# Performance work log

Measured on AMD Instinct MI355X. Metric: run time of the kernel, lower is better.

Reference implementation:

```python
import jax, jax.numpy as jnp
import numpy as np

B, S, H, NH = 2, 2048, 1024, 16
DH = H // NH
FF = 4 * H
EPS = 1e-5


def setup_inputs() -> dict:
    key = jax.random.key(0)
    ks = jax.random.split(key, 16)
    sd = 0.02
    inp = {
        "x": jax.random.normal(ks[0], (B, S, H), dtype=jnp.float32),
        "Wq": jax.random.normal(ks[1], (H, H), dtype=jnp.float32) * sd,
        "bq": jnp.zeros((H,), jnp.float32),
        "Wk": jax.random.normal(ks[2], (H, H), dtype=jnp.float32) * sd,
        "bk": jnp.zeros((H,), jnp.float32),
        "Wv": jax.random.normal(ks[3], (H, H), dtype=jnp.float32) * sd,
        "bv": jnp.zeros((H,), jnp.float32),
        "Wo": jax.random.normal(ks[4], (H, H), dtype=jnp.float32) * sd,
        "bo": jnp.zeros((H,), jnp.float32),
        "W1": jax.random.normal(ks[5], (H, FF), dtype=jnp.float32) * sd,
        "b1": jnp.zeros((FF,), jnp.float32),
        "W2": jax.random.normal(ks[6], (FF, H), dtype=jnp.float32) * sd,
        "b2": jnp.zeros((H,), jnp.float32),
        "g1": jnp.ones((H,), jnp.float32),
        "be1": jnp.zeros((H,), jnp.float32),
        "g2": jnp.ones((H,), jnp.float32),
        "be2": jnp.zeros((H,), jnp.float32),
    }
    return inp


def _layernorm(x, g, b):
    mu = jnp.mean(x, axis=-1, keepdims=True)
    var = jnp.mean(jnp.square(x - mu), axis=-1, keepdims=True)
    return (x - mu) * jax.lax.rsqrt(var + EPS) * g + b


def _block(x, Wq, bq, Wk, bk, Wv, bv, Wo, bo, W1, b1, W2, b2, g1, be1, g2, be2):
    # pre-LN attention
    h = _layernorm(x, g1, be1)
    q = (h @ Wq + bq).reshape(B, S, NH, DH)
    k = (h @ Wk + bk).reshape(B, S, NH, DH)
    v = (h @ Wv + bv).reshape(B, S, NH, DH)
    scale = DH ** -0.5
    scores = jnp.einsum("bqhd,bkhd->bhqk", q, k) * scale  # [B,NH,S,S]
    causal = jnp.tril(jnp.ones((S, S), dtype=bool))
    scores = jnp.where(causal, scores, -jnp.inf)
    attn = jax.nn.softmax(scores, axis=-1)
    out = jnp.einsum("bhqk,bkhd->bqhd", attn, v).reshape(B, S, H)
    x = x + (out @ Wo + bo)
    # pre-LN FFN with exact GELU (torch nn.GELU default)
    h = _layernorm(x, g2, be2)
    h = jax.nn.gelu(h @ W1 + b1, approximate=False)
    return x + (h @ W2 + b2)


def reference(x, Wq, bq, Wk, bk, Wv, bv, Wo, bo, W1, b1, W2, b2, g1, be1, g2, be2):
    return _block(x, Wq, bq, Wk, bk, Wv, bv, Wo, bo, W1, b1, W2, b2, g1, be1, g2, be2)
```

## Files before the change

### kernel.cpp

```cpp
#include <hip/hip_runtime.h>
#include <cstdint>
#include <cstddef>

typedef unsigned short u16;
typedef __attribute__((ext_vector_type(8))) __bf16 bf16v8;
typedef __attribute__((ext_vector_type(8))) unsigned short u16x8;
typedef __attribute__((ext_vector_type(4))) float f32x4;

constexpr int Bc = 2, Sc = 2048, Hc = 1024, NHc = 16, DHc = 64, FFc = 4096;
constexpr int Mc = Bc * Sc;

__device__ __forceinline__ u16 f2bf(float f) {
  unsigned u = __builtin_bit_cast(unsigned, f);
  return (u16)((u + 0x7FFFu + ((u >> 16) & 1u)) >> 16);
}

__device__ __forceinline__ int xcd_swz(int bid, int n) {
  const int q = n >> 3;
  return (bid & 7) * q + (bid >> 3);
}

__device__ __forceinline__ void gload_lds16(const void* g, void* l) {
  __builtin_amdgcn_global_load_lds(
      (const __attribute__((address_space(1))) unsigned*)(uintptr_t)g,
      (__attribute__((address_space(3))) unsigned*)(unsigned)(uintptr_t)l,
      16, 0, 0);
}

struct WP4 { const float* w0; const float* w1; const float* w2; const float* w3; };
__global__ __launch_bounds__(256) void wconv4_kernel(WP4 p, u16* __restrict__ Wt) {
  __shared__ float tile[64][65];
  const float* W = (blockIdx.z == 0) ? p.w0 : (blockIdx.z == 1) ? p.w1
                  : (blockIdx.z == 2) ? p.w2 : p.w3;
  u16* dst = Wt + (size_t)blockIdx.z * 1024 * 1024;
  const int n0 = blockIdx.x << 6, k0 = blockIdx.y << 6;
  const int t = threadIdx.x;
  const int col = t & 63, r0 = t >> 6;
#pragma unroll
  for (int i = 0; i < 16; ++i) {
    int r = (i << 2) + r0;
    tile[r][col] = W[(size_t)(k0 + r) * 1024 + n0 + col];
  }
  __syncthreads();
#pragma unroll
  for (int i = 0; i < 16; ++i) {
    int n = (i << 2) + r0;
    dst[(size_t)(n0 + n) * 1024 + k0 + col] = f2bf(tile[col][n]);
  }
}

struct WP2 { const float* w1; const float* w2; };
__global__ __launch_bounds__(256) void wconv12_kernel(WP2 p, u16* __restrict__ d1,
                                                      u16* __restrict__ d2) {
  __shared__ float tile[64][65];
  const int z = blockIdx.z;
  const float* W = z ? p.w2 : p.w1;
  u16* dst = z ? d2 : d1;
  const int K = z ? 4096 : 1024, N = z ? 1024 : 4096;
  const int nb = N >> 6;
  const int n0 = (blockIdx.x % nb) << 6, k0 = (blockIdx.x / nb) << 6;
  const int t = threadIdx.x;
  const int col = t & 63, r0 = t >> 6;
#pragma unroll
  for (int i = 0; i < 16; ++i) {
    int r = (i << 2) + r0;
    tile[r][col] = W[(size_t)(k0 + r) * N + n0 + col];
  }
  __syncthreads();
#pragma unroll
  for (int i = 0; i < 16; ++i) {
    int n = (i << 2) + r0;
    dst[(size_t)(n0 + n) * K + k0 + col] = f2bf(tile[col][n]);
  }
}

__global__ __launch_bounds__(256) void ln_kernel(const float* __restrict__ x,
                                                 const float* __restrict__ g,
                                                 const float* __restrict__ be,
                                                 u16* __restrict__ y) {
  const int row = blockIdx.x;
  const int t = threadIdx.x;
  const float4 v = ((const float4*)(x + (size_t)row * Hc))[t];
  float s1 = v.x + v.y + v.z + v.w;
  float s2 = v.x * v.x + v.y * v.y + v.z * v.z + v.w * v.w;
#pragma unroll
  for (int o = 32; o > 0; o >>= 1) {
    s1 += __shfl_xor(s1, o);
    s2 += __shfl_xor(s2, o);
  }
  __shared__ float r1[4], r2[4];
  const int wave = t >> 6, lane = t & 63;
  if (lane == 0) { r1[wave] = s1; r2[wave] = s2; }
  __syncthreads();
  s1 = r1[0] + r1[1] + r1[2] + r1[3];
  s2 = r2[0] + r2[1] + r2[2] + r2[3];
  const float mu = s1 * (1.f / Hc);
  const float var = s2 * (1.f / Hc) - mu * mu;
  const float rs = rsqrtf(var + 1e-5f);
  const float4 gv = ((const float4*)g)[t];
  const float4 bv = ((const float4*)be)[t];
  ushort4 ov;
  ov.x = f2bf((v.x - mu) * rs * gv.x + bv.x);
  ov.y = f2bf((v.y - mu) * rs * gv.y + bv.y);
  ov.z = f2bf((v.z - mu) * rs * gv.z + bv.z);
  ov.w = f2bf((v.w - mu) * rs * gv.w + bv.w);
  ((ushort4*)(y + (size_t)row * Hc))[t] = ov;
}

template <int EPI>
__global__ __launch_bounds__(256, 2) void gemm_kernel(
    const u16* __restrict__ A, const u16* __restrict__ Bt,
    const float* __restrict__ bias, const float* __restrict__ res,
    u16* __restrict__ outb, float* __restrict__ outf,
    int N, int Kext, int lda, int ldb, int nx) {
  __shared__ __align__(16) char smraw[32768];
  u16 (*As)[128][32] = (u16(*)[128][32])smraw;
  u16 (*Bs)[128][32] = (u16(*)[128][32])(smraw + 16384);
  float (*Cs)[16][132] = (float(*)[16][132])smraw;

  const int t = threadIdx.x;
  const int wave = t >> 6, lane = t & 63;
  const int pid = xcd_swz(blockIdx.x, gridDim.x);
  const int bn = pid % nx, bm = pid / nx;
  const int wm = wave >> 1, wn = wave & 1;
  const int fr = lane & 15, fk = (lane >> 4) << 3;

  f32x4 acc[4][4] = {};

  const int srow = (wave << 4) + (lane >> 2);
  const int scol = (lane & 3) << 3;
  const u16* Ag0 = A + (size_t)(bm * 128 + srow) * lda + scol;
  const u16* Ag1 = Ag0 + (size_t)64 * lda;
  const u16* Bg0 = Bt + (size_t)(bn * 128 + srow) * ldb + scol;
  const u16* Bg1 = Bg0 + (size_t)64 * ldb;

  const int nk = Kext >> 5;
  auto STAGE = [&](int buf, int k0) {
    gload_lds16(Ag0 + k0, &As[buf][wave << 4][0]);
    gload_lds16(Ag1 + k0, &As[buf][64 + (wave << 4)][0]);
    gload_lds16(Bg0 + k0, &Bs[buf][wave << 4][0]);
    gload_lds16(Bg1 + k0, &Bs[buf][64 + (wave << 4)][0]);
  };

  STAGE(0, 0);
  int cur = 0;
  for (int kt = 0; kt < nk; ++kt) {
    if (kt + 1 < nk) {
      STAGE(cur ^ 1, (kt + 1) << 5);
      asm volatile("s_waitcnt vmcnt(4)" ::: "memory");
    } else {
      asm volatile("s_waitcnt vmcnt(0)" ::: "memory");
    }
    __builtin_amdgcn_s_barrier();
    bf16v8 af[4], bfr[4];
#pragma unroll
    for (int i = 0; i < 4; ++i) af[i] = *(const bf16v8*)&As[cur][(wm << 6) + (i << 4) + fr][fk];
#pragma unroll
    for (int j = 0; j < 4; ++j) bfr[j] = *(const bf16v8*)&Bs[cur][(wn << 6) + (j << 4) + fr][fk];
    asm volatile("s_waitcnt lgkmcnt(0)" ::: "memory");
    __builtin_amdgcn_s_barrier();
    __builtin_amdgcn_s_setprio(1);
#pragma unroll
    for (int i = 0; i < 4; ++i)
#pragma unroll
      for (int j = 0; j < 4; ++j)
        acc[i][j] = __builtin_amdgcn_mfma_f32_16x16x32_bf16(af[i], bfr[j], acc[i][j], 0, 0, 0);
    __builtin_amdgcn_s_setprio(0);
    cur ^= 1;
  }
  __syncthreads();

  const int cr = (lane >> 4) << 2, cc = lane & 15;
  const int b2 = t >> 7, u = t & 127, lr = u >> 3, c0 = (u & 7) << 4;

  for (int i = 0; i < 4; ++i) {
#pragma unroll
    for (int j = 0; j < 4; ++j) {
      int col = (wn << 6) + (j << 4) + cc;
      float bz = bias[(bn << 7) + col];
#pragma unroll
      for (int r = 0; r < 4; ++r) Cs[wm][cr + r][col] = acc[i][j][r] + bz;
    }
    __syncthreads();
    {
      const float* crow = &Cs[b2][lr][c0];
      f32x4 v0 = *(const f32x4*)(crow);
      f32x4 v1 = *(const f32x4*)(crow + 4);
      f32x4 v2 = *(const f32x4*)(crow + 8);
      f32x4 v3 = *(const f32x4*)(crow + 12);
      const int grow = (bm << 7) + (b2 << 6) + (i << 4) + lr;
      const int gc = (bn << 7) + c0;
      const size_t base = (size_t)grow * N + gc;
      if constexpr (EPI == 0 || EPI == 1) {
        float vv[16];
#pragma unroll
        for (int k = 0; k < 4; ++k) { vv[k] = v0[k]; vv[4 + k] = v1[k]; vv[8 + k] = v2[k]; vv[12 + k] = v3[k]; }
        if constexpr (EPI == 1) {
#pragma unroll
          for (int k = 0; k < 16; ++k)
            vv[k] = 0.5f * vv[k] * (1.0f + erff(vv[k] * 0.70710678118654752f));
        }
        u16x8 o0, o1;
#pragma unroll
        for (int k = 0; k < 8; ++k) { o0[k] = f2bf(vv[k]); o1[k] = f2bf(vv[8 + k]); }
        *(u16x8*)&outb[base] = o0;
        *(u16x8*)&outb[base + 8] = o1;
      } else {
        const f32x4* rp = (const f32x4*)&res[base];
        v0 += rp[0]; v1 += rp[1]; v2 += rp[2]; v3 += rp[3];
        f32x4* op = (f32x4*)&outf[base];
        op[0] = v0; op[1] = v1; op[2] = v2; op[3] = v3;
      }
    }
    __syncthreads();
  }
}

template <int EPI>
__global__ __launch_bounds__(256, 2) void gemm_p_kernel(
    const u16* __restrict__ A, const u16* __restrict__ Bt,
    const float* __restrict__ bias, const float* __restrict__ res,
    u16* __restrict__ outb, float* __restrict__ outf,
    int N, int Kext, int lda, int ldb, int nx) {
  __shared__ __align__(16) char smraw[49152];
  u16 (*As)[128][32] = (u16(*)[128][32])smraw;
  u16 (*Bs)[128][32] = (u16(*)[128][32])(smraw + 24576);
  float (*Cs)[16][132] = (float(*)[16][132])smraw;

  const int t = threadIdx.x;
  const int wave = t >> 6, lane = t & 63;
  const int pid = xcd_swz(blockIdx.x, gridDim.x);
  const int bn = pid % nx, bm = pid / nx;
  const int wm = wave >> 1, wn = wave & 1;
  const int fr = lane & 15, fk = (lane >> 4) << 3;

  f32x4 acc[4][4] = {};

  const int srow = (wave << 4) + (lane >> 2);
  const int scol = (lane & 3) << 3;
  const u16* Ag0 = A + (size_t)(bm * 128 + srow) * lda + scol;
  const u16* Ag1 = Ag0 + (size_t)64 * lda;
  const u16* Bg0 = Bt + (size_t)(bn * 128 + srow) * ldb + scol;
  const u16* Bg1 = Bg0 + (size_t)64 * ldb;

  const int nk = Kext >> 5;
  auto STAGE = [&](int buf, int k0) {
    gload_lds16(Ag0 + k0, &As[buf][wave << 4][0]);
    gload_lds16(Ag1 + k0, &As[buf][64 + (wave << 4)][0]);
    gload_lds16(Bg0 + k0, &Bs[buf][wave << 4][0]);
    gload_lds16(Bg1 + k0, &Bs[buf][64 + (wave << 4)][0]);
  };

  STAGE(0, 0);
  STAGE(1, 32);
  int cur = 0;
  for (int kt = 0; kt < nk; ++kt) {
    if (kt + 2 < nk) {
      int sb = cur + 2; if (sb >= 3) sb -= 3;
      STAGE(sb, (kt + 2) << 5);
      asm volatile("s_waitcnt vmcnt(8)" ::: "memory");
    } else if (kt + 1 < nk) {
      asm volatile("s_waitcnt vmcnt(4)" ::: "memory");
    } else {
      asm volatile("s_waitcnt vmcnt(0)" ::: "memory");
    }
    __builtin_amdgcn_s_barrier();
    bf16v8 af[4], bfr[4];
#pragma unroll
    for (int i = 0; i < 4; ++i) af[i] = *(const bf16v8*)&As[cur][(wm << 6) + (i << 4) + fr][fk];
#pragma unroll
    for (int j = 0; j < 4; ++j) bfr[j] = *(const bf16v8*)&Bs[cur][(wn << 6) + (j << 4) + fr][fk];
    asm volatile("s_waitcnt lgkmcnt(0)" ::: "memory");
    __builtin_amdgcn_s_barrier();
    __builtin_amdgcn_s_setprio(1);
#pragma unroll
    for (int i = 0; i < 4; ++i)
#pragma unroll
      for (int j = 0; j < 4; ++j)
        acc[i][j] = __builtin_amdgcn_mfma_f32_16x16x32_bf16(af[i], bfr[j], acc[i][j], 0, 0, 0);
    __builtin_amdgcn_s_setprio(0);
    cur = (cur + 1 == 3) ? 0 : cur + 1;
  }
  __syncthreads();

  const int cr = (lane >> 4) << 2, cc = lane & 15;
  const int b2 = t >> 7, u = t & 127, lr = u >> 3, c0 = (u & 7) << 4;

  for (int i = 0; i < 4; ++i) {
#pragma unroll
    for (int j = 0; j < 4; ++j) {
      int col = (wn << 6) + (j << 4) + cc;
      float bz = bias[(bn << 7) + col];
#pragma unroll
      for (int r = 0; r < 4; ++r) Cs[wm][cr + r][col] = acc[i][j][r] + bz;
    }
    __syncthreads();
    {
      const float* crow = &Cs[b2][lr][c0];
      f32x4 v0 = *(const f32x4*)(crow);
      f32x4 v1 = *(const f32x4*)(crow + 4);
      f32x4 v2 = *(const f32x4*)(crow + 8);
      f32x4 v3 = *(const f32x4*)(crow + 12);
      const int grow = (bm << 7) + (b2 << 6) + (i << 4) + lr;
      const int gc = (bn << 7) + c0;
      const size_t base = (size_t)grow * N + gc;
      if constexpr (EPI == 0 || EPI == 1) {
        float vv[16];
#pragma unroll
        for (int k = 0; k < 4; ++k) { vv[k] = v0[k]; vv[4 + k] = v1[k]; vv[8 + k] = v2[k]; vv[12 + k] = v3[k]; }
        if constexpr (EPI == 1) {
#pragma unroll
          for (int k = 0; k < 16; ++k)
            vv[k] = 0.5f * vv[k] * (1.0f + erff(vv[k] * 0.70710678118654752f));
        }
        u16x8 o0, o1;
#pragma unroll
        for (int k = 0; k < 8; ++k) { o0[k] = f2bf(vv[k]); o1[k] = f2bf(vv[8 + k]); }
        *(u16x8*)&outb[base] = o0;
        *(u16x8*)&outb[base + 8] = o1;
      } else {
        const f32x4* rp = (const f32x4*)&res[base];
        v0 += rp[0]; v1 += rp[1]; v2 += rp[2]; v3 += rp[3];
        f32x4* op = (f32x4*)&outf[base];
        op[0] = v0; op[1] = v1; op[2] = v2; op[3] = v3;
      }
    }
    __syncthreads();
  }
}

__global__ __launch_bounds__(256, 2) void qkv_gemm_kernel(
    const u16* __restrict__ A, const u16* __restrict__ Bt,
    const float* __restrict__ bq, const float* __restrict__ bk,
    const float* __restrict__ bv,
    u16* __restrict__ Qb, u16* __restrict__ Kb, u16* __restrict__ Vtg) {
  constexpr int K = 1024;
  __shared__ __align__(16) char smraw[49152];
  u16 (*As)[128][32] = (u16(*)[128][32])smraw;
  u16 (*Bs)[128][32] = (u16(*)[128][32])(smraw + 24576);
  float (*Cs)[16][132] = (float(*)[16][132])smraw;

  const int t = threadIdx.x;
  const int wave = t >> 6, lane = t & 63;
  const int pid = xcd_swz(blockIdx.x, 768);
  const int bn = pid % 24, bm = pid / 24;
  const int wm = wave >> 1, wn = wave & 1;
  const int fr = lane & 15, fk = (lane >> 4) << 3;
  const int seg = bn >> 3;

  f32x4 acc[4][4] = {};

  const int srow = (wave << 4) + (lane >> 2);
  const int scol = (lane & 3) << 3;
  const u16* Ag0 = A + (size_t)(bm * 128 + srow) * K + scol;
  const u16* Ag1 = Ag0 + (size_t)64 * K;
  const u16* Bg0 = Bt + (size_t)(bn * 128 + srow) * K + scol;
  const u16* Bg1 = Bg0 + (size_t)64 * K;

  const int nk = K >> 5;
  auto STAGE = [&](int buf, int k0) {
    gload_lds16(Ag0 + k0, &As[buf][wave << 4][0]);
    gload_lds16(Ag1 + k0, &As[buf][64 + (wave << 4)][0]);
    gload_lds16(Bg0 + k0, &Bs[buf][wave << 4][0]);
    gload_lds16(Bg1 + k0, &Bs[buf][64 + (wave << 4)][0]);
  };

  STAGE(0, 0);
  STAGE(1, 32);
  int cur = 0;
  for (int kt = 0; kt < nk; ++kt) {
    if (kt + 2 < nk) {
      int sb = cur + 2; if (sb >= 3) sb -= 3;
      STAGE(sb, (kt + 2) << 5);
      asm volatile("s_waitcnt vmcnt(8)" ::: "memory");
    } else if (kt + 1 < nk) {
      asm volatile("s_waitcnt vmcnt(4)" ::: "memory");
    } else {
      asm volatile("s_waitcnt vmcnt(0)" ::: "memory");
    }
    __builtin_amdgcn_s_barrier();
    bf16v8 af[4], bfr[4];
#pragma unroll
    for (int i = 0; i < 4; ++i) af[i] = *(const bf16v8*)&As[cur][(wm << 6) + (i << 4) + fr][fk];
#pragma unroll
    for (int j = 0; j < 4; ++j) bfr[j] = *(const bf16v8*)&Bs[cur][(wn << 6) + (j << 4) + fr][fk];
    asm volatile("s_waitcnt lgkmcnt(0)" ::: "memory");
    __builtin_amdgcn_s_barrier();
    __builtin_amdgcn_s_setprio(1);
#pragma unroll
    for (int i = 0; i < 4; ++i)
#pragma unroll
      for (int j = 0; j < 4; ++j)
        acc[i][j] = __builtin_amdgcn_mfma_f32_16x16x32_bf16(af[i], bfr[j], acc[i][j], 0, 0, 0);
    __builtin_amdgcn_s_setprio(0);
    cur = (cur + 1 == 3) ? 0 : cur + 1;
  }
  __syncthreads();

  const int cr = (lane >> 4) << 2, cc = lane & 15;
  const int b2 = t >> 7, u = t & 127, lr = u >> 3, c0 = (u & 7) << 4;
  const float* bp = (seg == 0) ? bq : (seg == 1) ? bk : bv;

  for (int i = 0; i < 4; ++i) {
#pragma unroll
    for (int j = 0; j < 4; ++j) {
      int col = (wn << 6) + (j << 4) + cc;
      float bz = bp[((bn << 7) + col) & 1023];
#pragma unroll
      for (int r = 0; r < 4; ++r) Cs[wm][cr + r][col] = acc[i][j][r] + bz;
    }
    __syncthreads();
    if (seg < 2) {
      const float* crow = &Cs[b2][lr][c0];
      f32x4 v0 = *(const f32x4*)(crow);
      f32x4 v1 = *(const f32x4*)(crow + 4);
      f32x4 v2 = *(const f32x4*)(crow + 8);
      f32x4 v3 = *(const f32x4*)(crow + 12);
      const int grow = (bm << 7) + (b2 << 6) + (i << 4) + lr;
      const int cn0 = (((bn & 7) << 7) + c0);
      u16* dst = (seg == 0) ? Qb : Kb;
      u16x8 o0, o1;
#pragma unroll
      for (int k = 0; k < 4; ++k) {
        o0[k] = f2bf(v0[k]); o0[4 + k] = f2bf(v1[k]);
        o1[k] = f2bf(v2[k]); o1[4 + k] = f2bf(v3[k]);
      }
      *(u16x8*)&dst[(size_t)grow * 1024 + cn0] = o0;
      *(u16x8*)&dst[(size_t)grow * 1024 + cn0 + 8] = o1;
    } else {
      const int cv = ((bn & 7) << 7) + u;
      const int h = cv >> 6, dh = cv & 63;
#pragma unroll
      for (int oct = 0; oct < 2; ++oct) {
        u16x8 o;
#pragma unroll
        for (int k = 0; k < 8; ++k) o[k] = f2bf(Cs[b2][(oct << 3) + k][u]);
        const int srow2 = (bm << 7) + (b2 << 6) + (i << 4) + (oct << 3);
        const int bb = srow2 >> 11, s = srow2 & 2047;
        size_t idx = ((size_t)(bb * 16 + h)) * (64 * 2048) + (size_t)dh * 2048 + s;
        *(u16x8*)&Vtg[idx] = o;
      }
    }
    __syncthreads();
  }
}

__global__ __launch_bounds__(256, 3) void attn_kernel(const u16* __restrict__ Q,
                                                      const u16* __restrict__ Kb,
                                                      const u16* __restrict__ Vt,
                                                      u16* __restrict__ O) {
  constexpr float CS = 0.18033688011112042f;
  constexpr float M2 = 8.0f;
  const int pid = xcd_swz(blockIdx.x, 512);
  const int bx = pid & 15, bh = pid >> 4;
  const int t = threadIdx.x, wave = t >> 6, lane = t & 63;
  const int fr = lane & 15, fk = (lane >> 4) << 3;

  __shared__ u16 Ks[2][64][72];
  __shared__ u16 Vs[2][64][72];
  __shared__ u16 Ps[4][16][72];

  const size_t base = ((size_t)(bh >> 4) * Sc) * Hc + (bh & 15) * DHc;
  const u16* Qp = Q + base;
  const u16* Kp = Kb + base;
  const u16* Vp = Vt + (size_t)bh * (64 * 2048);

  const int r_st = t >> 3;
  const int co_st = (t & 7) << 3;

  bf16v8 ones;
#pragma unroll
  for (int k = 0; k < 8; ++k) ones[k] = (__bf16)1.0f;

  for (int half = 0; half < 2; ++half) {
    const int qt = half ? (31 - bx) : bx;
    const int q0 = qt << 6;
    const int nt = qt + 1;

    const int qrow = q0 + (wave << 4) + fr;
    const bf16v8 qf0 = *(const bf16v8*)&Qp[(size_t)qrow * Hc + fk];
    const bf16v8 qf1 = *(const bf16v8*)&Qp[(size_t)qrow * Hc + 32 + fk];

    f32x4 oacc[4] = {};
    f32x4 osum = {};

    const int crow0 = q0 + (wave << 4) + ((lane >> 4) << 2);

    u16x8 rk0, rk1, rv0, rv1;
    auto LD = [&](int kv0) {
      rk0 = *(const u16x8*)&Kp[(size_t)(kv0 + r_st) * Hc + co_st];
      rk1 = *(const u16x8*)&Kp[(size_t)(kv0 + 32 + r_st) * Hc + co_st];
      rv0 = *(const u16x8*)&Vp[(size_t)r_st * 2048 + kv0 + co_st];
      rv1 = *(const u16x8*)&Vp[(size_t)(32 + r_st) * 2048 + kv0 + co_st];
    };
    auto WR = [&](int buf) {
      *(u16x8*)&Ks[buf][r_st][co_st] = rk0;
      *(u16x8*)&Ks[buf][32 + r_st][co_st] = rk1;
      *(u16x8*)&Vs[buf][r_st][co_st] = rv0;
      *(u16x8*)&Vs[buf][32 + r_st][co_st] = rv1;
    };

    LD(0);
    WR(0);
    __syncthreads();
    int cur = 0;
    for (int it = 0; it < nt; ++it) {
      const int kv0 = it << 6;
      const bool hasnext = (it + 1 < nt);
      if (hasnext) LD(kv0 + 64);

      f32x4 sc[4];
      __builtin_amdgcn_s_setprio(1);
#pragma unroll
      for (int c = 0; c < 4; ++c) {
        bf16v8 kf0 = *(const bf16v8*)&Ks[cur][(c << 4) + fr][fk];
        bf16v8 kf1 = *(const bf16v8*)&Ks[cur][(c << 4) + fr][32 + fk];
        f32x4 a = {0.f, 0.f, 0.f, 0.f};
        a = __builtin_amdgcn_mfma_f32_16x16x32_bf16(qf0, kf0, a, 0, 0, 0);
        a = __builtin_amdgcn_mfma_f32_16x16x32_bf16(qf1, kf1, a, 0, 0, 0);
        sc[c] = a;
      }
      __builtin_amdgcn_s_setprio(0);

      if (kv0 + 64 > q0) {
#pragma unroll
        for (int c = 0; c < 4; ++c)
#pragma unroll
          for (int r = 0; r < 4; ++r) {
            int kv = kv0 + (c << 4) + fr;
            if (kv > crow0 + r) sc[c][r] = -INFINITY;
          }
      }

#pragma unroll
      for (int c = 0; c < 4; ++c)
#pragma unroll
        for (int r = 0; r < 4; ++r) {
          float p = exp2f(fmaf(sc[c][r], CS, -M2));
          Ps[wave][((lane >> 4) << 2) + r][(c << 4) + fr] = f2bf(p);
        }

      const bf16v8 pa0 = *(const bf16v8*)&Ps[wave][fr][fk];
      const bf16v8 pa1 = *(const bf16v8*)&Ps[wave][fr][32 + fk];
      __builtin_amdgcn_s_setprio(1);
#pragma unroll
      for (int f = 0; f < 4; ++f) {
        bf16v8 vf0 = *(const bf16v8*)&Vs[cur][(f << 4) + fr][fk];
        bf16v8 vf1 = *(const bf16v8*)&Vs[cur][(f << 4) + fr][32 + fk];
        oacc[f] = __builtin_amdgcn_mfma_f32_16x16x32_bf16(pa0, vf0, oacc[f], 0, 0, 0);
        oacc[f] = __builtin_amdgcn_mfma_f32_16x16x32_bf16(pa1, vf1, oacc[f], 0, 0, 0);
      }
      osum = __builtin_amdgcn_mfma_f32_16x16x32_bf16(pa0, ones, osum, 0, 0, 0);
      osum = __builtin_amdgcn_mfma_f32_16x16x32_bf16(pa1, ones, osum, 0, 0, 0);
      __builtin_amdgcn_s_setprio(0);

      if (hasnext) WR(cur ^ 1);
      __syncthreads();
      cur ^= 1;
    }
#pragma unroll
    for (int r = 0; r < 4; ++r) {
      float inv = 1.0f / osum[r];
      int row = crow0 + r;
#pragma unroll
      for (int f = 0; f < 4; ++f)
        O[base + (size_t)row * Hc + (f << 4) + fr] = f2bf(oacc[f][r] * inv);
    }
    __syncthreads();
  }
}

extern "C" void kernel_launch(void* const* d_in, const int* in_sizes, int n_in,
                              void* d_out, int out_size, void* d_ws, size_t ws_size,
                              hipStream_t stream) {
  const float* x  = (const float*)d_in[0];
  const float* Wq = (const float*)d_in[1];
  const float* bq = (const float*)d_in[2];
  const float* Wk = (const float*)d_in[3];
  const float* bk = (const float*)d_in[4];
  const float* Wv = (const float*)d_in[5];
  const float* bv = (const float*)d_in[6];
  const float* Wo = (const float*)d_in[7];
  const float* bo = (const float*)d_in[8];
  const float* W1 = (const float*)d_in[9];
  const float* b1 = (const float*)d_in[10];
  const float* W2 = (const float*)d_in[11];
  const float* b2 = (const float*)d_in[12];
  const float* g1 = (const float*)d_in[13];
  const float* be1 = (const float*)d_in[14];
  const float* g2 = (const float*)d_in[15];
  const float* be2 = (const float*)d_in[16];
  float* out = (float*)d_out;

  char* ws = (char*)d_ws;
  const size_t MB = 1024 * 1024;
  u16* wqkv = (u16*)(ws + 0 * MB);
  u16* wo   = (u16*)(ws + 6 * MB);
  u16* w1   = (u16*)(ws + 8 * MB);
  u16* w2   = (u16*)(ws + 16 * MB);
  u16* lnb  = (u16*)(ws + 24 * MB);
  u16* Qb   = (u16*)(ws + 32 * MB);
  u16* Kb   = (u16*)(ws + 40 * MB);
  u16* Vtg  = (u16*)(ws + 48 * MB);
  u16* Ob   = (u16*)(ws + 56 * MB);
  u16* H1   = (u16*)(ws + 32 * MB);

  dim3 blk(256);
  WP4 wp{Wq, Wk, Wv, Wo};
  wconv4_kernel<<<dim3(16, 16, 4), blk, 0, stream>>>(wp, wqkv);
  WP2 wp2{W1, W2};
  wconv12_kernel<<<dim3(1024, 1, 2), blk, 0, stream>>>(wp2, w1, w2);

  ln_kernel<<<Mc, blk, 0, stream>>>(x, g1, be1, lnb);

  qkv_gemm_kernel<<<dim3(768), blk, 0, stream>>>(lnb, wqkv, bq, bk, bv, Qb, Kb, Vtg);

  attn_kernel<<<dim3(512), blk, 0, stream>>>(Qb, Kb, Vtg, Ob);

  gemm_p_kernel<2><<<dim3(256), blk, 0, stream>>>(Ob, wo, bo, x, nullptr, out,
                                                  1024, 1024, 1024, 1024, 8);

  ln_kernel<<<Mc, blk, 0, stream>>>(out, g2, be2, lnb);

  gemm_kernel<1><<<dim3(1024), blk, 0, stream>>>(lnb, w1, b1, nullptr, H1, nullptr,
                                                 4096, 1024, 1024, 1024, 32);

  gemm_p_kernel<2><<<dim3(256), blk, 0, stream>>>(H1, w2, b2, out, nullptr, out,
                                                  1024, 4096, 4096, 4096, 8);
}
```

Baseline: 247.1 us.

## Widen attention blocks to 128 query rows and merge weight conversion kernels

The attention kernel now runs 512 threads (8 waves) per block, each block covering 128 query rows per half instead of 64. Every K/V tile loaded into shared memory is therefore reused by twice as many waves, which halves global K/V traffic per query. The cost is more fully masked causal work for the early waves and half as many blocks to spread across CUs. Separately, the two fp32-to-bf16 weight transpose launches are merged into one six-slice launch to save a kernel launch; the square-weight slices exit early for most of their blocks.

```diff
diff --git a/kernel.cpp b/kernel.cpp
--- a/kernel.cpp
+++ b/kernel.cpp
@@ -27,38 +27,29 @@
       16, 0, 0);
 }
 
-struct WP4 { const float* w0; const float* w1; const float* w2; const float* w3; };
-__global__ __launch_bounds__(256) void wconv4_kernel(WP4 p, u16* __restrict__ Wt) {
-  __shared__ float tile[64][65];
-  const float* W = (blockIdx.z == 0) ? p.w0 : (blockIdx.z == 1) ? p.w1
-                  : (blockIdx.z == 2) ? p.w2 : p.w3;
-  u16* dst = Wt + (size_t)blockIdx.z * 1024 * 1024;
-  const int n0 = blockIdx.x << 6, k0 = blockIdx.y << 6;
-  const int t = threadIdx.x;
-  const int col = t & 63, r0 = t >> 6;
-#pragma unroll
-  for (int i = 0; i < 16; ++i) {
-    int r = (i << 2) + r0;
-    tile[r][col] = W[(size_t)(k0 + r) * 1024 + n0 + col];
-  }
-  __syncthreads();
-#pragma unroll
-  for (int i = 0; i < 16; ++i) {
-    int n = (i << 2) + r0;
-    dst[(size_t)(n0 + n) * 1024 + k0 + col] = f2bf(tile[col][n]);
-  }
-}
-
-struct WP2 { const float* w1; const float* w2; };
-__global__ __launch_bounds__(256) void wconv12_kernel(WP2 p, u16* __restrict__ d1,
-                                                      u16* __restrict__ d2) {
+struct WP6 { const float* wq; const float* wk; const float* wv; const float* wo;
+             const float* w1; const float* w2; };
+__global__ __launch_bounds__(256) void wconv_all_kernel(WP6 p, u16* __restrict__ wqkv,
+                                                        u16* __restrict__ d1,
+                                                        u16* __restrict__ d2) {
   __shared__ float tile[64][65];
   const int z = blockIdx.z;
-  const float* W = z ? p.w2 : p.w1;
-  u16* dst = z ? d2 : d1;
-  const int K = z ? 4096 : 1024, N = z ? 1024 : 4096;
+  const int bid = blockIdx.x;
+  const float* W;
+  u16* dst;
+  int K, N;
+  if (z < 4) {
+    if (bid >= 256) return;
+    W = (z == 0) ? p.wq : (z == 1) ? p.wk : (z == 2) ? p.wv : p.wo;
+    dst = wqkv + ((size_t)z << 20);
+    K = 1024; N = 1024;
+  } else if (z == 4) {
+    W = p.w1; dst = d1; K = 1024; N = 4096;
+  } else {
+    W = p.w2; dst = d2; K = 4096; N = 1024;
+  }
   const int nb = N >> 6;
-  const int n0 = (blockIdx.x % nb) << 6, k0 = (blockIdx.x / nb) << 6;
+  const int n0 = (bid % nb) << 6, k0 = (bid / nb) << 6;
   const int t = threadIdx.x;
   const int col = t & 63, r0 = t >> 6;
 #pragma unroll
@@ -445,20 +436,20 @@
   }
 }
 
-__global__ __launch_bounds__(256, 3) void attn_kernel(const u16* __restrict__ Q,
+__global__ __launch_bounds__(512, 2) void attn_kernel(const u16* __restrict__ Q,
                                                       const u16* __restrict__ Kb,
                                                       const u16* __restrict__ Vt,
                                                       u16* __restrict__ O) {
   constexpr float CS = 0.18033688011112042f;
   constexpr float M2 = 8.0f;
-  const int pid = xcd_swz(blockIdx.x, 512);
-  const int bx = pid & 15, bh = pid >> 4;
+  const int pid = xcd_swz(blockIdx.x, 256);
+  const int bx = pid & 7, bh = pid >> 3;
   const int t = threadIdx.x, wave = t >> 6, lane = t & 63;
   const int fr = lane & 15, fk = (lane >> 4) << 3;
 
   __shared__ u16 Ks[2][64][72];
   __shared__ u16 Vs[2][64][72];
-  __shared__ u16 Ps[4][16][72];
+  __shared__ u16 Ps[8][16][72];
 
   const size_t base = ((size_t)(bh >> 4) * Sc) * Hc + (bh & 15) * DHc;
   const u16* Qp = Q + base;
@@ -473,9 +464,9 @@
   for (int k = 0; k < 8; ++k) ones[k] = (__bf16)1.0f;
 
   for (int half = 0; half < 2; ++half) {
-    const int qt = half ? (31 - bx) : bx;
-    const int q0 = qt << 6;
-    const int nt = qt + 1;
+    const int QT = half ? (15 - bx) : bx;
+    const int q0 = QT << 7;
+    const int nt = (QT + 1) << 1;
 
     const int qrow = q0 + (wave << 4) + fr;
     const bf16v8 qf0 = *(const bf16v8*)&Qp[(size_t)qrow * Hc + fk];
@@ -486,18 +477,14 @@
 
     const int crow0 = q0 + (wave << 4) + ((lane >> 4) << 2);
 
-    u16x8 rk0, rk1, rv0, rv1;
+    u16x8 rk, rv;
     auto LD = [&](int kv0) {
-      rk0 = *(const u16x8*)&Kp[(size_t)(kv0 + r_st) * Hc + co_st];
-      rk1 = *(const u16x8*)&Kp[(size_t)(kv0 + 32 + r_st) * Hc + co_st];
-      rv0 = *(const u16x8*)&Vp[(size_t)r_st * 2048 + kv0 + co_st];
-      rv1 = *(const u16x8*)&Vp[(size_t)(32 + r_st) * 2048 + kv0 + co_st];
+      rk = *(const u16x8*)&Kp[(size_t)(kv0 + r_st) * Hc + co_st];
+      rv = *(const u16x8*)&Vp[(size_t)r_st * 2048 + kv0 + co_st];
     };
     auto WR = [&](int buf) {
-      *(u16x8*)&Ks[buf][r_st][co_st] = rk0;
-      *(u16x8*)&Ks[buf][32 + r_st][co_st] = rk1;
-      *(u16x8*)&Vs[buf][r_st][co_st] = rv0;
-      *(u16x8*)&Vs[buf][32 + r_st][co_st] = rv1;
+      *(u16x8*)&Ks[buf][r_st][co_st] = rk;
+      *(u16x8*)&Vs[buf][r_st][co_st] = rv;
     };
 
     LD(0);
@@ -606,16 +593,14 @@
   u16* H1   = (u16*)(ws + 32 * MB);
 
   dim3 blk(256);
-  WP4 wp{Wq, Wk, Wv, Wo};
-  wconv4_kernel<<<dim3(16, 16, 4), blk, 0, stream>>>(wp, wqkv);
-  WP2 wp2{W1, W2};
-  wconv12_kernel<<<dim3(1024, 1, 2), blk, 0, stream>>>(wp2, w1, w2);
+  WP6 wp{Wq, Wk, Wv, Wo, W1, W2};
+  wconv_all_kernel<<<dim3(1024, 1, 6), blk, 0, stream>>>(wp, wqkv, w1, w2);
 
   ln_kernel<<<Mc, blk, 0, stream>>>(x, g1, be1, lnb);
 
   qkv_gemm_kernel<<<dim3(768), blk, 0, stream>>>(lnb, wqkv, bq, bk, bv, Qb, Kb, Vtg);
 
-  attn_kernel<<<dim3(512), blk, 0, stream>>>(Qb, Kb, Vtg, Ob);
+  attn_kernel<<<dim3(256), dim3(512), 0, stream>>>(Qb, Kb, Vtg, Ob);
 
   gemm_p_kernel<2><<<dim3(256), blk, 0, stream>>>(Ob, wo, bo, x, nullptr, out,
                                                   1024, 1024, 1024, 1024, 8);
```

New measurement: 241.8 us (median of 2 runs). 1.02x faster.
